# Optimization experiments

Measured on AMD Instinct MI355X. Metric: run time of the kernel, lower is better.

## Reference

```python
import jax, jax.numpy as jnp
import numpy as np
from jax import lax

B, C_IN, H, W = 32, 3, 224, 224
EMBED = 768 // 4  # dim // 4 = 192
K = 3             # kernel_size
STRIDE = 2        # patch_stride
PAD = 1           # patch_padding
BN_EPS = 1e-5


def setup_inputs() -> dict:
    key = jax.random.key(0)
    kx, kw, kb, kg, kbeta = jax.random.split(key, 5)
    x = jax.random.normal(kx, (B, C_IN, H, W), dtype=jnp.float32)
    fan_in = C_IN * K * K
    bound = 1.0 / np.sqrt(fan_in)
    conv_w = jax.random.uniform(kw, (EMBED, C_IN, K, K), jnp.float32, -bound, bound)
    conv_b = jax.random.uniform(kb, (EMBED,), jnp.float32, -bound, bound)
    gamma = jnp.ones((EMBED,), jnp.float32)
    beta = jnp.zeros((EMBED,), jnp.float32)
    return {"x": x, "conv_w": conv_w, "conv_b": conv_b, "gamma": gamma, "beta": beta}


def _patch_embed(x, conv_w, conv_b, gamma, beta):
    # Conv2d(in_chans, embed_dim, k=3, stride=2, pad=1)
    y = lax.conv_general_dilated(
        x, conv_w,
        window_strides=(STRIDE, STRIDE),
        padding=[(PAD, PAD), (PAD, PAD)],
        dimension_numbers=("NCHW", "OIHW", "NCHW"),
    ) + conv_b[None, :, None, None]  # [B, EMBED, 112, 112]
    # BatchNorm2d (training mode: batch statistics, biased variance)
    mean = jnp.mean(y, axis=(0, 2, 3), keepdims=True)
    var = jnp.mean(jnp.square(y - mean), axis=(0, 2, 3), keepdims=True)
    y = (y - mean) * lax.rsqrt(var + BN_EPS)
    y = y * gamma[None, :, None, None] + beta[None, :, None, None]
    # GELU (torch default: exact erf form)
    y = jax.nn.gelu(y, approximate=False)
    # MaxPool2d(kernel=3, stride=2, padding=1)
    y = lax.reduce_window(
        y, -jnp.inf, lax.max,
        window_dimensions=(1, 1, 3, 3),
        window_strides=(1, 1, STRIDE, STRIDE),
        padding=[(0, 0), (0, 0), (PAD, PAD), (PAD, PAD)],
    )  # [B, EMBED, 56, 56]
    return y


def reference(x, conv_w, conv_b, gamma, beta):
    return _patch_embed(x, conv_w, conv_b, gamma, beta)
```

## Files before the change

kernel.cpp:

```cpp
#include <hip/hip_runtime.h>
#include <hip/hip_bf16.h>
#include <math.h>

#define B_   32
#define CIN  3
#define H_   224
#define W_   224
#define OC   192
#define OH   112
#define OW   112
#define PH   56
#define PW   56
#define NSP  (B_*OH*OW)
#define PLANE (OH*OW)
#define LROW 116
#define LPAD 8

static __device__ __forceinline__ unsigned short f2bf(float f) {
    __hip_bfloat16 h = __float2bfloat16(f);
    return *reinterpret_cast<unsigned short*>(&h);
}
static __device__ __forceinline__ float bfbits2f(unsigned short u) {
    unsigned int v = ((unsigned int)u) << 16;
    return *reinterpret_cast<float*>(&v);
}

static __device__ __forceinline__ float fexp2(float x) {
#if __has_builtin(__builtin_amdgcn_exp2f)
    return __builtin_amdgcn_exp2f(x);
#else
    return exp2f(x);
#endif
}
static __device__ __forceinline__ float frcp(float x) {
#if __has_builtin(__builtin_amdgcn_rcpf)
    return __builtin_amdgcn_rcpf(x);
#else
    return 1.0f / x;
#endif
}

static __device__ __forceinline__ float fast_gelu(float x) {
    float x2 = x * x;
    float inner = fmaf(0.044715f * x2, x, x);
    float e = fexp2(inner * 2.3022082f);
    float r = frcp(1.0f + e);
    return x * (e * r);
}

__global__ void zero_stats(float* stats) {
    for (int i = threadIdx.x; i < 768; i += 256) stats[i] = 0.f;
}

__global__ __launch_bounds__(256) void conv_kernel(
    const float* __restrict__ x, const float* __restrict__ w,
    const float* __restrict__ bias, __hip_bfloat16* __restrict__ y)
{
    int g = blockIdx.x * 256 + threadIdx.x;
    int owg = g % (OW / 4);
    int t   = g / (OW / 4);
    int oh  = t % OH;
    int b   = t / OH;
    int ow0 = owg * 4;

    int ih0 = 2 * oh  - 1;
    int iw0 = 2 * ow0 - 1;

    float xv[CIN][3][9];
    #pragma unroll
    for (int c = 0; c < CIN; ++c) {
        #pragma unroll
        for (int r = 0; r < 3; ++r) {
            int ih = ih0 + r;
            bool rv = (ih >= 0) && (ih < H_);
            const float* xrow = x + (((size_t)b * CIN + c) * H_ + (rv ? ih : 0)) * W_;
            #pragma unroll
            for (int j = 0; j < 9; ++j) {
                int iw = iw0 + j;
                bool v = rv && (iw >= 0) && (iw < W_);
                xv[c][r][j] = v ? xrow[iw] : 0.f;
            }
        }
    }

    int ybase = (b * OC) * PLANE + oh * OW + ow0;

    for (int oc = 0; oc < OC; ++oc) {
        float bs = bias[oc];
        float a0 = bs, a1 = bs, a2 = bs, a3 = bs;
        const float* wp = w + oc * 27;
        #pragma unroll
        for (int c = 0; c < CIN; ++c)
            #pragma unroll
            for (int r = 0; r < 3; ++r)
                #pragma unroll
                for (int j = 0; j < 3; ++j) {
                    float wv = wp[c * 9 + r * 3 + j];
                    a0 = fmaf(wv, xv[c][r][j + 0], a0);
                    a1 = fmaf(wv, xv[c][r][j + 2], a1);
                    a2 = fmaf(wv, xv[c][r][j + 4], a2);
                    a3 = fmaf(wv, xv[c][r][j + 6], a3);
                }
        ushort4 p;
        p.x = f2bf(a0); p.y = f2bf(a1); p.z = f2bf(a2); p.w = f2bf(a3);
        *reinterpret_cast<ushort4*>(
            reinterpret_cast<unsigned short*>(y) + ybase + oc * PLANE) = p;
    }
}

__global__ __launch_bounds__(256) void stats_kernel(
    const __hip_bfloat16* __restrict__ y, float* __restrict__ stats)
{
    int plane = blockIdx.x;
    int oc = plane % OC;
    const unsigned int* p =
        reinterpret_cast<const unsigned int*>(y) + plane * (PLANE / 2);

    float s = 0.f, s2 = 0.f;
    for (int ch = threadIdx.x; ch < PLANE / 8; ch += 256) {
        uint4 v = reinterpret_cast<const uint4*>(p)[ch];
        unsigned int u[4] = {v.x, v.y, v.z, v.w};
        #pragma unroll
        for (int k = 0; k < 4; ++k) {
            float lo = bfbits2f((unsigned short)(u[k] & 0xffffu));
            float hi = bfbits2f((unsigned short)(u[k] >> 16));
            s  += lo + hi;
            s2 += lo * lo + hi * hi;
        }
    }

    __shared__ float ls[256], ls2[256];
    int tid = threadIdx.x;
    ls[tid] = s; ls2[tid] = s2;
    __syncthreads();
    for (int off = 128; off > 0; off >>= 1) {
        if (tid < off) { ls[tid] += ls[tid + off]; ls2[tid] += ls2[tid + off]; }
        __syncthreads();
    }
    if (tid == 0) {
        atomicAdd(&stats[oc], ls[0]);
        atomicAdd(&stats[192 + oc], ls2[0]);
    }
}

__global__ __launch_bounds__(448) void pool_kernel(
    const __hip_bfloat16* __restrict__ y, const float* __restrict__ stats,
    const float* __restrict__ gamma, const float* __restrict__ beta,
    float* __restrict__ out)
{
    __shared__ float g[LPAD + OH * LROW];

    int plane = blockIdx.x;
    int oc = plane % OC;

    float mean = stats[oc] * (1.0f / (float)NSP);
    float var  = fmaf(-mean, mean, stats[192 + oc] * (1.0f / (float)NSP));
    float inv  = rsqrtf(var + 1e-5f);
    float sc   = gamma[oc] * inv;
    float sh   = fmaf(-mean, sc, beta[oc]);

    const uint2* p = reinterpret_cast<const uint2*>(
        reinterpret_cast<const unsigned short*>(y) + (size_t)plane * PLANE);

    int t = threadIdx.x;
    #pragma unroll
    for (int it = 0; it < 7; ++it) {
        int gi = it * 448 + t;
        uint2 v = p[gi];
        int row = gi / 28;
        int col = (gi - row * 28) * 4;
        float4 q;
        q.x = fast_gelu(fmaf(bfbits2f((unsigned short)(v.x & 0xffffu)), sc, sh));
        q.y = fast_gelu(fmaf(bfbits2f((unsigned short)(v.x >> 16)),     sc, sh));
        q.z = fast_gelu(fmaf(bfbits2f((unsigned short)(v.y & 0xffffu)), sc, sh));
        q.w = fast_gelu(fmaf(bfbits2f((unsigned short)(v.y >> 16)),     sc, sh));
        *reinterpret_cast<float4*>(&g[LPAD + row * LROW + col]) = q;
    }
    __syncthreads();

    int r = t >> 3;
    int k = t & 7;
    int c0 = 14 * k - 2;

    float vm[16];
    #pragma unroll
    for (int q = 0; q < 16; ++q) vm[q] = -INFINITY;

    #pragma unroll
    for (int rr = 0; rr < 3; ++rr) {
        int row = 2 * r - 1 + rr;
        if (row < 0) continue;
        const float2* rp = reinterpret_cast<const float2*>(&g[LPAD + row * LROW + c0]);
        #pragma unroll
        for (int q = 0; q < 8; ++q) {
            float2 v = rp[q];
            vm[2 * q]     = fmaxf(vm[2 * q],     v.x);
            vm[2 * q + 1] = fmaxf(vm[2 * q + 1], v.y);
        }
    }
    if (k == 0) vm[1] = -INFINITY;

    float* op = out + (size_t)plane * (PH * PW) + r * PW + 7 * k;
    #pragma unroll
    for (int m = 0; m < 7; ++m) {
        op[m] = fmaxf(fmaxf(vm[2 * m + 1], vm[2 * m + 2]), vm[2 * m + 3]);
    }
}

extern "C" void kernel_launch(void* const* d_in, const int* in_sizes, int n_in,
                              void* d_out, int out_size, void* d_ws, size_t ws_size,
                              hipStream_t stream) {
    const float* x     = (const float*)d_in[0];
    const float* w     = (const float*)d_in[1];
    const float* bias  = (const float*)d_in[2];
    const float* gamma = (const float*)d_in[3];
    const float* beta  = (const float*)d_in[4];
    float* out = (float*)d_out;

    float* stats = (float*)d_ws;
    __hip_bfloat16* y = (__hip_bfloat16*)((char*)d_ws + 4096);

    hipLaunchKernelGGL(zero_stats, dim3(1), dim3(256), 0, stream, stats);
    hipLaunchKernelGGL(conv_kernel, dim3((B_ * OH * (OW / 4)) / 256), dim3(256), 0, stream,
                       x, w, bias, y);
    hipLaunchKernelGGL(stats_kernel, dim3(B_ * OC), dim3(256), 0, stream, y, stats);
    hipLaunchKernelGGL(pool_kernel, dim3(B_ * OC), dim3(448), 0, stream,
                       y, stats, gamma, beta, out);
}
```

Before: 239.3 us.

## Fuse BN statistics into conv kernel and split output channels across blocks

Computes per-channel sum and sum-of-squares inside the conv kernel with wave shuffles and shared-memory reduction, then atomically adds them, which removes the separate stats pass that re-read the whole bf16 intermediate. The grid is also split into 8 channel groups per spatial tile to raise parallelism. In exchange the input patch loads are repeated for each group, and the number of atomics grows. Statistics are now computed from fp32 accumulators rather than the bf16-rounded values.

```diff
diff --git a/kernel.cpp b/kernel.cpp
--- a/kernel.cpp
+++ b/kernel.cpp
@@ -15,6 +15,8 @@
 #define PLANE (OH*OW)
 #define LROW 116
 #define LPAD 8
+#define OCG  8
+#define OCPG (OC / OCG)
 
 static __device__ __forceinline__ unsigned short f2bf(float f) {
     __hip_bfloat16 h = __float2bfloat16(f);
@@ -49,16 +51,24 @@
 }
 
 __global__ void zero_stats(float* stats) {
-    for (int i = threadIdx.x; i < 768; i += 256) stats[i] = 0.f;
+    for (int i = threadIdx.x; i < 384; i += 256) stats[i] = 0.f;
 }
 
 __global__ __launch_bounds__(256) void conv_kernel(
     const float* __restrict__ x, const float* __restrict__ w,
-    const float* __restrict__ bias, __hip_bfloat16* __restrict__ y)
+    const float* __restrict__ bias, __hip_bfloat16* __restrict__ y,
+    float* __restrict__ stats)
 {
-    int g = blockIdx.x * 256 + threadIdx.x;
-    int owg = g % (OW / 4);
-    int t   = g / (OW / 4);
+    __shared__ float lsum[4][OCPG][2];
+
+    int gb = blockIdx.x;
+    int og = gb & (OCG - 1);
+    int sp = gb >> 3;
+    int tid = threadIdx.x;
+
+    int spatial = sp * 256 + tid;
+    int owg = spatial % (OW / 4);
+    int t   = spatial / (OW / 4);
     int oh  = t % OH;
     int b   = t / OH;
     int ow0 = owg * 4;
@@ -83,9 +93,13 @@
         }
     }
 
-    int ybase = (b * OC) * PLANE + oh * OW + ow0;
-
-    for (int oc = 0; oc < OC; ++oc) {
+    int oc0 = og * OCPG;
+    int ybase = (b * OC + oc0) * PLANE + oh * OW + ow0;
+    int wave = tid >> 6;
+    int lane = tid & 63;
+
+    for (int ocl = 0; ocl < OCPG; ++ocl) {
+        int oc = oc0 + ocl;
         float bs = bias[oc];
         float a0 = bs, a1 = bs, a2 = bs, a3 = bs;
         const float* wp = w + oc * 27;
@@ -101,45 +115,28 @@
                     a2 = fmaf(wv, xv[c][r][j + 4], a2);
                     a3 = fmaf(wv, xv[c][r][j + 6], a3);
                 }
+
+        float s  = (a0 + a1) + (a2 + a3);
+        float s2 = fmaf(a0, a0, fmaf(a1, a1, fmaf(a2, a2, a3 * a3)));
+        #pragma unroll
+        for (int off = 32; off > 0; off >>= 1) {
+            s  += __shfl_xor(s,  off, 64);
+            s2 += __shfl_xor(s2, off, 64);
+        }
+        if (lane == 0) { lsum[wave][ocl][0] = s; lsum[wave][ocl][1] = s2; }
+
         ushort4 p;
         p.x = f2bf(a0); p.y = f2bf(a1); p.z = f2bf(a2); p.w = f2bf(a3);
         *reinterpret_cast<ushort4*>(
-            reinterpret_cast<unsigned short*>(y) + ybase + oc * PLANE) = p;
-    }
-}
-
-__global__ __launch_bounds__(256) void stats_kernel(
-    const __hip_bfloat16* __restrict__ y, float* __restrict__ stats)
-{
-    int plane = blockIdx.x;
-    int oc = plane % OC;
-    const unsigned int* p =
-        reinterpret_cast<const unsigned int*>(y) + plane * (PLANE / 2);
-
-    float s = 0.f, s2 = 0.f;
-    for (int ch = threadIdx.x; ch < PLANE / 8; ch += 256) {
-        uint4 v = reinterpret_cast<const uint4*>(p)[ch];
-        unsigned int u[4] = {v.x, v.y, v.z, v.w};
-        #pragma unroll
-        for (int k = 0; k < 4; ++k) {
-            float lo = bfbits2f((unsigned short)(u[k] & 0xffffu));
-            float hi = bfbits2f((unsigned short)(u[k] >> 16));
-            s  += lo + hi;
-            s2 += lo * lo + hi * hi;
-        }
-    }
-
-    __shared__ float ls[256], ls2[256];
-    int tid = threadIdx.x;
-    ls[tid] = s; ls2[tid] = s2;
+            reinterpret_cast<unsigned short*>(y) + ybase + ocl * PLANE) = p;
+    }
+
     __syncthreads();
-    for (int off = 128; off > 0; off >>= 1) {
-        if (tid < off) { ls[tid] += ls[tid + off]; ls2[tid] += ls2[tid + off]; }
-        __syncthreads();
-    }
-    if (tid == 0) {
-        atomicAdd(&stats[oc], ls[0]);
-        atomicAdd(&stats[192 + oc], ls2[0]);
+    if (tid < OCPG * 2) {
+        int ocl = tid >> 1, which = tid & 1;
+        float v = lsum[0][ocl][which] + lsum[1][ocl][which] +
+                  lsum[2][ocl][which] + lsum[3][ocl][which];
+        atomicAdd(&stats[which * OC + oc0 + ocl], v);
     }
 }
 
@@ -154,7 +151,7 @@
     int oc = plane % OC;
 
     float mean = stats[oc] * (1.0f / (float)NSP);
-    float var  = fmaf(-mean, mean, stats[192 + oc] * (1.0f / (float)NSP));
+    float var  = fmaf(-mean, mean, stats[OC + oc] * (1.0f / (float)NSP));
     float inv  = rsqrtf(var + 1e-5f);
     float sc   = gamma[oc] * inv;
     float sh   = fmaf(-mean, sc, beta[oc]);
@@ -221,9 +218,8 @@
     __hip_bfloat16* y = (__hip_bfloat16*)((char*)d_ws + 4096);
 
     hipLaunchKernelGGL(zero_stats, dim3(1), dim3(256), 0, stream, stats);
-    hipLaunchKernelGGL(conv_kernel, dim3((B_ * OH * (OW / 4)) / 256), dim3(256), 0, stream,
-                       x, w, bias, y);
-    hipLaunchKernelGGL(stats_kernel, dim3(B_ * OC), dim3(256), 0, stream, y, stats);
+    hipLaunchKernelGGL(conv_kernel, dim3((B_ * OH * (OW / 4)) / 256 * OCG), dim3(256), 0,
+                       stream, x, w, bias, y, stats);
     hipLaunchKernelGGL(pool_kernel, dim3(B_ * OC), dim3(448), 0, stream,
                        y, stats, gamma, beta, out);
 }
```

Measured after the change: 258.9 us. +8.2%, slower.

## Split conv output channels across blocks and pool before normalize+GELU via min/max

Applied to the files above, without the earlier changes.

The conv kernel now splits the 192 output channels into 8 groups across separate blocks. That gives 8x more blocks for parallelism, and each block recomputes its input patch. The pool kernel drops the shared-memory plane staging: each thread reads its own 3x3 window of raw bf16 values and tracks min and max. It then applies the affine BN and GELU only to those two extremes. This relies on the affine map being monotone (either sign) and GELU being unimodal, so the max of GELU over the window falls at one of the endpoints. The goal is to cut GELU evaluations and shared-memory traffic, at the cost of uncoalesced, redundant global reads.

```diff
diff --git a/kernel.cpp b/kernel.cpp
--- a/kernel.cpp
+++ b/kernel.cpp
@@ -13,8 +13,8 @@
 #define PW   56
 #define NSP  (B_*OH*OW)
 #define PLANE (OH*OW)
-#define LROW 116
-#define LPAD 8
+#define OCG  8
+#define OCPG (OC / OCG)
 
 static __device__ __forceinline__ unsigned short f2bf(float f) {
     __hip_bfloat16 h = __float2bfloat16(f);
@@ -49,16 +49,21 @@
 }
 
 __global__ void zero_stats(float* stats) {
-    for (int i = threadIdx.x; i < 768; i += 256) stats[i] = 0.f;
+    for (int i = threadIdx.x; i < 384; i += 256) stats[i] = 0.f;
 }
 
 __global__ __launch_bounds__(256) void conv_kernel(
     const float* __restrict__ x, const float* __restrict__ w,
     const float* __restrict__ bias, __hip_bfloat16* __restrict__ y)
 {
-    int g = blockIdx.x * 256 + threadIdx.x;
-    int owg = g % (OW / 4);
-    int t   = g / (OW / 4);
+    int gb = blockIdx.x;
+    int og = gb & (OCG - 1);
+    int sp = gb >> 3;
+    int tid = threadIdx.x;
+
+    int spatial = sp * 256 + tid;
+    int owg = spatial % (OW / 4);
+    int t   = spatial / (OW / 4);
     int oh  = t % OH;
     int b   = t / OH;
     int ow0 = owg * 4;
@@ -83,12 +88,13 @@
         }
     }
 
-    int ybase = (b * OC) * PLANE + oh * OW + ow0;
-
-    for (int oc = 0; oc < OC; ++oc) {
-        float bs = bias[oc];
+    int oc0 = og * OCPG;
+    int ybase = (b * OC + oc0) * PLANE + oh * OW + ow0;
+
+    for (int ocl = 0; ocl < OCPG; ++ocl) {
+        float bs = bias[oc0 + ocl];
         float a0 = bs, a1 = bs, a2 = bs, a3 = bs;
-        const float* wp = w + oc * 27;
+        const float* wp = w + (oc0 + ocl) * 27;
         #pragma unroll
         for (int c = 0; c < CIN; ++c)
             #pragma unroll
@@ -104,7 +110,7 @@
         ushort4 p;
         p.x = f2bf(a0); p.y = f2bf(a1); p.z = f2bf(a2); p.w = f2bf(a3);
         *reinterpret_cast<ushort4*>(
-            reinterpret_cast<unsigned short*>(y) + ybase + oc * PLANE) = p;
+            reinterpret_cast<unsigned short*>(y) + ybase + ocl * PLANE) = p;
     }
 }
 
@@ -139,72 +145,53 @@
     }
     if (tid == 0) {
         atomicAdd(&stats[oc], ls[0]);
-        atomicAdd(&stats[192 + oc], ls2[0]);
-    }
-}
-
-__global__ __launch_bounds__(448) void pool_kernel(
+        atomicAdd(&stats[OC + oc], ls2[0]);
+    }
+}
+
+__global__ __launch_bounds__(256) void pool_kernel(
     const __hip_bfloat16* __restrict__ y, const float* __restrict__ stats,
     const float* __restrict__ gamma, const float* __restrict__ beta,
     float* __restrict__ out)
 {
-    __shared__ float g[LPAD + OH * LROW];
-
-    int plane = blockIdx.x;
-    int oc = plane % OC;
+    int g = blockIdx.x * 256 + threadIdx.x;
+    int pw = g % PW;
+    int t  = g / PW;
+    int ph = t % PH;
+    t /= PH;
+    int oc = t % OC;
+    int b  = t / OC;
+
+    const unsigned short* p =
+        reinterpret_cast<const unsigned short*>(y) + (size_t)(b * OC + oc) * PLANE;
+
+    float vmax = -INFINITY, vmin = INFINITY;
+    #pragma unroll
+    for (int rr = 0; rr < 3; ++rr) {
+        int ih = 2 * ph - 1 + rr;
+        bool rv = (ih >= 0) && (ih < OH);
+        const unsigned short* rowp = p + (rv ? ih : 0) * OW;
+        #pragma unroll
+        for (int jj = 0; jj < 3; ++jj) {
+            int iw = 2 * pw - 1 + jj;
+            bool v = rv && (iw >= 0) && (iw < OW);
+            if (v) {
+                float f = bfbits2f(rowp[iw]);
+                vmax = fmaxf(vmax, f);
+                vmin = fminf(vmin, f);
+            }
+        }
+    }
 
     float mean = stats[oc] * (1.0f / (float)NSP);
-    float var  = fmaf(-mean, mean, stats[192 + oc] * (1.0f / (float)NSP));
+    float var  = fmaf(-mean, mean, stats[OC + oc] * (1.0f / (float)NSP));
     float inv  = rsqrtf(var + 1e-5f);
     float sc   = gamma[oc] * inv;
     float sh   = fmaf(-mean, sc, beta[oc]);
 
-    const uint2* p = reinterpret_cast<const uint2*>(
-        reinterpret_cast<const unsigned short*>(y) + (size_t)plane * PLANE);
-
-    int t = threadIdx.x;
-    #pragma unroll
-    for (int it = 0; it < 7; ++it) {
-        int gi = it * 448 + t;
-        uint2 v = p[gi];
-        int row = gi / 28;
-        int col = (gi - row * 28) * 4;
-        float4 q;
-        q.x = fast_gelu(fmaf(bfbits2f((unsigned short)(v.x & 0xffffu)), sc, sh));
-        q.y = fast_gelu(fmaf(bfbits2f((unsigned short)(v.x >> 16)),     sc, sh));
-        q.z = fast_gelu(fmaf(bfbits2f((unsigned short)(v.y & 0xffffu)), sc, sh));
-        q.w = fast_gelu(fmaf(bfbits2f((unsigned short)(v.y >> 16)),     sc, sh));
-        *reinterpret_cast<float4*>(&g[LPAD + row * LROW + col]) = q;
-    }
-    __syncthreads();
-
-    int r = t >> 3;
-    int k = t & 7;
-    int c0 = 14 * k - 2;
-
-    float vm[16];
-    #pragma unroll
-    for (int q = 0; q < 16; ++q) vm[q] = -INFINITY;
-
-    #pragma unroll
-    for (int rr = 0; rr < 3; ++rr) {
-        int row = 2 * r - 1 + rr;
-        if (row < 0) continue;
-        const float2* rp = reinterpret_cast<const float2*>(&g[LPAD + row * LROW + c0]);
-        #pragma unroll
-        for (int q = 0; q < 8; ++q) {
-            float2 v = rp[q];
-            vm[2 * q]     = fmaxf(vm[2 * q],     v.x);
-            vm[2 * q + 1] = fmaxf(vm[2 * q + 1], v.y);
-        }
-    }
-    if (k == 0) vm[1] = -INFINITY;
-
-    float* op = out + (size_t)plane * (PH * PW) + r * PW + 7 * k;
-    #pragma unroll
-    for (int m = 0; m < 7; ++m) {
-        op[m] = fmaxf(fmaxf(vm[2 * m + 1], vm[2 * m + 2]), vm[2 * m + 3]);
-    }
+    float lo = fmaf(vmin, sc, sh);
+    float hi = fmaf(vmax, sc, sh);
+    out[g] = fmaxf(fast_gelu(lo), fast_gelu(hi));
 }
 
 extern "C" void kernel_launch(void* const* d_in, const int* in_sizes, int n_in,
@@ -221,9 +208,9 @@
     __hip_bfloat16* y = (__hip_bfloat16*)((char*)d_ws + 4096);
 
     hipLaunchKernelGGL(zero_stats, dim3(1), dim3(256), 0, stream, stats);
-    hipLaunchKernelGGL(conv_kernel, dim3((B_ * OH * (OW / 4)) / 256), dim3(256), 0, stream,
-                       x, w, bias, y);
+    hipLaunchKernelGGL(conv_kernel, dim3((B_ * OH * (OW / 4)) / 256 * OCG), dim3(256), 0,
+                       stream, x, w, bias, y);
     hipLaunchKernelGGL(stats_kernel, dim3(B_ * OC), dim3(256), 0, stream, y, stats);
-    hipLaunchKernelGGL(pool_kernel, dim3(B_ * OC), dim3(448), 0, stream,
+    hipLaunchKernelGGL(pool_kernel, dim3((B_ * OC * PH * PW) / 256), dim3(256), 0, stream,
                        y, stats, gamma, beta, out);
 }
```

After: 379.0 us. 58.4% more time.
